# Kernel optimization log

Measured on AMD Instinct MI355X. Metric: run time of the kernel, lower is better.

## Reference

```python
import jax, jax.numpy as jnp
import numpy as np

B, D, H = 4096, 1024, 1024


def setup_inputs() -> dict:
    key = jax.random.key(0)
    ks = jax.random.split(key, 20)
    s_in = 1.0 / np.sqrt(D)
    s_hid = 1.0 / np.sqrt(H)
    inp = {
        "x_t": jax.random.normal(ks[0], (B, D), dtype=jnp.float32),
        "h_t_1": jax.random.normal(ks[1], (B, H), dtype=jnp.float32),
        "c_t_1": jax.random.normal(ks[2], (B, H), dtype=jnp.float32),
        # input-to-hidden weights (nn.Linear: y = x @ W.T + b), stacked i,f,o,z
        "W": jax.random.uniform(ks[3], (4, H, D), minval=-s_in, maxval=s_in, dtype=jnp.float32),
        "bW": jax.random.uniform(ks[4], (4, H), minval=-s_in, maxval=s_in, dtype=jnp.float32),
        # hidden-to-hidden weights, stacked i,f,o,z
        "U": jax.random.uniform(ks[5], (4, H, H), minval=-s_hid, maxval=s_hid, dtype=jnp.float32),
        "bU": jax.random.uniform(ks[6], (4, H), minval=-s_hid, maxval=s_hid, dtype=jnp.float32),
    }
    return inp


def reference(x_t, h_t_1, c_t_1, W, bW, U, bU):
    # Two stacked GEMMs: [B,D]x[4,H,D] -> [4,B,H], [B,H]x[4,H,H] -> [4,B,H]
    gx = jnp.einsum("bd,ghd->gbh", x_t, W) + bW[:, None, :]
    gh = jnp.einsum("bh,gkh->gbk", h_t_1, U) + bU[:, None, :]
    g = gx + gh  # [4, B, H] pre-activations for i, f, o, z
    i = jax.nn.sigmoid(g[0])
    f = jax.nn.sigmoid(g[1])
    o = jax.nn.sigmoid(g[2])
    z = jnp.tanh(g[3])
    c_t = i * z + f * c_t_1
    h_t = o * jnp.tanh(c_t)
    return (h_t, c_t)
```

## Files before the change

kernel.cpp:

```cpp
#include <hip/hip_runtime.h>
#include <math.h>

#define Mm 4096
#define Nn 4096
#define Kk 2048

typedef __bf16 bf16x8 __attribute__((ext_vector_type(8)));
typedef float f32x4 __attribute__((ext_vector_type(4)));

__device__ __forceinline__ unsigned short f2bf(float f) {
    union { float f; unsigned u; } v; v.f = f;
    unsigned r = v.u + 0x7FFFu + ((v.u >> 16) & 1u);
    return (unsigned short)(r >> 16);
}

__device__ __forceinline__ float fast_tanh(float x) {
    return 1.f - 2.f / (1.f + __expf(2.f * x));
}

__global__ void pack_bf16(const float* __restrict__ x, const float* __restrict__ h,
                          const float* __restrict__ W, const float* __restrict__ U,
                          const float* __restrict__ bW, const float* __restrict__ bU,
                          unsigned short* __restrict__ Xc, unsigned short* __restrict__ Wc,
                          float* __restrict__ bsum) {
    if (blockIdx.x == 0) {
#pragma unroll
        for (int j = 0; j < 16; ++j) {
            int n = threadIdx.x * 16 + j;
            int hh = n >> 2, g = n & 3;
            bsum[n] = bW[g * 1024 + hh] + bU[g * 1024 + hh];
        }
    }
    const int PER = (4096 * 1024) / 4;
    for (int t = blockIdx.x * blockDim.x + threadIdx.x; t < 4 * PER;
         t += gridDim.x * blockDim.x) {
        int region = t >> 20;
        int i = t & (PER - 1);
        int row = i >> 8;
        int c4  = i & 255;
        const float* src = (region == 0) ? x : (region == 1) ? h : (region == 2) ? W : U;
        float4 v = reinterpret_cast<const float4*>(src)[i];
        ushort4 o;
        o.x = f2bf(v.x); o.y = f2bf(v.y); o.z = f2bf(v.z); o.w = f2bf(v.w);
        if (region < 2) {
            *reinterpret_cast<ushort4*>(Xc + (size_t)row * 2048 + (region << 10) + c4 * 4) = o;
        } else {
            int g = row >> 10, hh = row & 1023;
            int np = ((hh >> 4) << 6) + (g << 4) + (hh & 15);
            *reinterpret_cast<ushort4*>(Wc + (size_t)np * 2048 + ((region & 1) << 10) + c4 * 4) = o;
        }
    }
}

__device__ __forceinline__ void gl16(const void* g, void* l) {
    __builtin_amdgcn_global_load_lds(
        (const __attribute__((address_space(1))) void*)g,
        (__attribute__((address_space(3))) void*)l, 16, 0, 0);
}

#define A_OFF(p, ah) (((p) * 2 + (ah)) * 16384)
#define B_OFF(p, hb) (65536 + ((p) * 2 + (hb)) * 16384)

__global__ __launch_bounds__(512, 2) void gemm_8ph(const unsigned short* __restrict__ A,
                                                   const unsigned short* __restrict__ Bw,
                                                   const float* __restrict__ bsum,
                                                   const float* __restrict__ cprev,
                                                   float* __restrict__ out) {
    extern __shared__ char lds[];
    const int tid = threadIdx.x, lane = tid & 63, wave = tid >> 6;
    const int wm = wave >> 2, wn = wave & 3;

    const int bid = blockIdx.x;
    const int swz = (bid & 7) * 32 + (bid >> 3);
    const int bm = swz & 15, bn = swz >> 4;
    const size_t Crow0 = (size_t)bm * 256, Ccol0 = (size_t)bn * 256;

    const int srow = wave * 8 + (lane >> 3);
    const int scolswz = (((lane & 7) ^ (lane >> 3)) << 4);
    const char* aS[2][2];
    const char* bS[2][2];
#pragma unroll
    for (int ah = 0; ah < 2; ++ah)
#pragma unroll
        for (int j = 0; j < 2; ++j) {
            aS[ah][j] = (const char*)A  + (size_t)(Crow0 + ah * 128 + j * 64 + srow) * 4096 + scolswz;
            bS[ah][j] = (const char*)Bw + (size_t)(Ccol0 + ah * 128 + j * 64 + srow) * 4096 + scolswz;
        }

#define STG_A(p, ah, kb) do { \
        gl16(aS[ah][0] + (kb), lds + A_OFF(p, ah) + wave * 1024); \
        gl16(aS[ah][1] + (kb), lds + A_OFF(p, ah) + 8192 + wave * 1024); } while (0)
#define STG_B(p, hb, kb) do { \
        gl16(bS[hb][0] + (kb), lds + B_OFF(p, hb) + wave * 1024); \
        gl16(bS[hb][1] + (kb), lds + B_OFF(p, hb) + 8192 + wave * 1024); } while (0)

    const int arowB = (wm * 64 + (lane & 15)) * 128;
    const int browB = ((wn & 1) * 64 + (lane & 15)) * 128;
    const int c0 = (((lane >> 4) << 4)) ^ ((lane & 7) << 4);
    const int c1 = (64 + ((lane >> 4) << 4)) ^ ((lane & 7) << 4);
    const int bhb = wn >> 1;

#define LDA(p, ah, mfl, ck) (*(const bf16x8*)(lds + A_OFF(p, ah) + arowB + (mfl) * 2048 + (ck)))
#define LDB(p, nf, ck)      (*(const bf16x8*)(lds + B_OFF(p, bhb) + browB + (nf) * 2048 + (ck)))

    f32x4 acc[2][4][4] = {};

#define MFMA(a, b, c) __builtin_amdgcn_mfma_f32_16x16x32_bf16(a, b, c, 0, 0, 0)
#define MF16(ah, mfA, mfB, p00, p01, p10, p11) \
    acc[ah][mfA][0] = MFMA(p00, b00, acc[ah][mfA][0]); \
    acc[ah][mfA][1] = MFMA(p00, b10, acc[ah][mfA][1]); \
    acc[ah][mfA][2] = MFMA(p00, b20, acc[ah][mfA][2]); \
    acc[ah][mfA][3] = MFMA(p00, b30, acc[ah][mfA][3]); \
    acc[ah][mfB][0] = MFMA(p10, b00, acc[ah][mfB][0]); \
    acc[ah][mfB][1] = MFMA(p10, b10, acc[ah][mfB][1]); \
    acc[ah][mfB][2] = MFMA(p10, b20, acc[ah][mfB][2]); \
    acc[ah][mfB][3] = MFMA(p10, b30, acc[ah][mfB][3]); \
    acc[ah][mfA][0] = MFMA(p01, b01, acc[ah][mfA][0]); \
    acc[ah][mfA][1] = MFMA(p01, b11, acc[ah][mfA][1]); \
    acc[ah][mfA][2] = MFMA(p01, b21, acc[ah][mfA][2]); \
    acc[ah][mfA][3] = MFMA(p01, b31, acc[ah][mfA][3]); \
    acc[ah][mfB][0] = MFMA(p11, b01, acc[ah][mfB][0]); \
    acc[ah][mfB][1] = MFMA(p11, b11, acc[ah][mfB][1]); \
    acc[ah][mfB][2] = MFMA(p11, b21, acc[ah][mfB][2]); \
    acc[ah][mfB][3] = MFMA(p11, b31, acc[ah][mfB][3]);

#define PH_TAIL \
    __builtin_amdgcn_s_barrier(); \
    asm volatile("s_waitcnt lgkmcnt(0)" ::: "memory"); \
    __builtin_amdgcn_s_setprio(1);

#define PH_END \
    __builtin_amdgcn_s_setprio(0); \
    __builtin_amdgcn_s_barrier();

#define GROUP(p, kbA1, kbT2) \
    { \
        bf16x8 b00 = LDB(p, 0, c0), b01 = LDB(p, 0, c1), b10 = LDB(p, 1, c0), b11 = LDB(p, 1, c1); \
        bf16x8 b20 = LDB(p, 2, c0), b21 = LDB(p, 2, c1), b30 = LDB(p, 3, c0), b31 = LDB(p, 3, c1); \
        {  \
            bf16x8 a00 = LDA(p, 0, 0, c0), a01 = LDA(p, 0, 0, c1); \
            bf16x8 a10 = LDA(p, 0, 1, c0), a11 = LDA(p, 0, 1, c1); \
            STG_A((p) ^ 1, 1, kbA1); \
            PH_TAIL MF16(0, 0, 1, a00, a01, a10, a11) PH_END \
        } \
        {  \
            bf16x8 a00 = LDA(p, 0, 2, c0), a01 = LDA(p, 0, 2, c1); \
            bf16x8 a10 = LDA(p, 0, 3, c0), a11 = LDA(p, 0, 3, c1); \
            STG_B(p, 0, kbT2); \
            PH_TAIL MF16(0, 2, 3, a00, a01, a10, a11) PH_END \
        } \
        {  \
            bf16x8 a00 = LDA(p, 1, 0, c0), a01 = LDA(p, 1, 0, c1); \
            bf16x8 a10 = LDA(p, 1, 1, c0), a11 = LDA(p, 1, 1, c1); \
            STG_A(p, 0, kbT2); \
            PH_TAIL MF16(1, 0, 1, a00, a01, a10, a11) PH_END \
        } \
        {  \
            bf16x8 a00 = LDA(p, 1, 2, c0), a01 = LDA(p, 1, 2, c1); \
            bf16x8 a10 = LDA(p, 1, 3, c0), a11 = LDA(p, 1, 3, c1); \
            STG_B(p, 1, kbT2); \
            __builtin_amdgcn_s_barrier(); \
            asm volatile("s_waitcnt lgkmcnt(0)" ::: "memory"); \
            __builtin_amdgcn_s_setprio(1); \
            MF16(1, 2, 3, a00, a01, a10, a11) \
            __builtin_amdgcn_s_setprio(0); \
            asm volatile("s_waitcnt vmcnt(6)" ::: "memory"); \
            __builtin_amdgcn_s_barrier(); \
        } \
    }

    STG_B(0, 0, 0);
    STG_A(0, 0, 0);
    STG_B(0, 1, 0);
    STG_A(0, 1, 0);
    STG_B(1, 0, 128);
    STG_A(1, 0, 128);
    STG_B(1, 1, 128);
    asm volatile("s_waitcnt vmcnt(6)" ::: "memory");
    __builtin_amdgcn_s_barrier();

    for (int it = 0; it < 16; ++it) {
        const int t0 = 2 * it;
        const size_t kA1_0 = (size_t)(t0 + 1) * 128;
        const size_t kT2_0 = (t0 + 2 <= 31) ? (size_t)(t0 + 2) * 128 : 0;
        const size_t kA1_1 = kT2_0;
        const size_t kT2_1 = (t0 + 3 <= 31) ? (size_t)(t0 + 3) * 128 : 0;
        GROUP(0, kA1_0, kT2_0)
        GROUP(1, kA1_1, kT2_1)
    }

    const int hl = lane & 15;
    const int er0 = (lane >> 4) * 4;
    const int myh = (int)(Ccol0 >> 2) + wn * 16 + hl;
    const f32x4 bs = *(const f32x4*)(bsum + (size_t)myh * 4);

    float cp[2][4][4];
#pragma unroll
    for (int ah = 0; ah < 2; ++ah)
#pragma unroll
        for (int mf = 0; mf < 4; ++mf)
#pragma unroll
            for (int r = 0; r < 4; ++r)
                cp[ah][mf][r] = cprev[(size_t)(Crow0 + ah * 128 + wm * 64 + mf * 16 + er0 + r) * 1024 + myh];

#pragma unroll
    for (int ah = 0; ah < 2; ++ah)
#pragma unroll
        for (int mf = 0; mf < 4; ++mf)
#pragma unroll
            for (int r = 0; r < 4; ++r) {
                float gi = acc[ah][mf][0][r] + bs[0];
                float gf = acc[ah][mf][1][r] + bs[1];
                float go = acc[ah][mf][2][r] + bs[2];
                float gz = acc[ah][mf][3][r] + bs[3];
                float iv = 1.f / (1.f + __expf(-gi));
                float fv = 1.f / (1.f + __expf(-gf));
                float ov = 1.f / (1.f + __expf(-go));
                float zv = fast_tanh(gz);
                float cc = fmaf(iv, zv, fv * cp[ah][mf][r]);
                float hv = ov * fast_tanh(cc);
                const size_t oidx =
                    (size_t)(Crow0 + ah * 128 + wm * 64 + mf * 16 + er0 + r) * 1024 + myh;
                out[oidx] = hv;
                out[(1 << 22) + oidx] = cc;
            }

    asm volatile("s_waitcnt vmcnt(0)" ::: "memory");
}

extern "C" void kernel_launch(void* const* d_in, const int* in_sizes, int n_in,
                              void* d_out, int out_size, void* d_ws, size_t ws_size,
                              hipStream_t stream) {
    const float* x  = (const float*)d_in[0];
    const float* h  = (const float*)d_in[1];
    const float* c  = (const float*)d_in[2];
    const float* W  = (const float*)d_in[3];
    const float* bW = (const float*)d_in[4];
    const float* U  = (const float*)d_in[5];
    const float* bU = (const float*)d_in[6];
    float* out = (float*)d_out;

    char* ws = (char*)d_ws;
    unsigned short* Xc = (unsigned short*)ws;
    unsigned short* Wc = (unsigned short*)(ws + ((size_t)16 << 20));
    float* bsum = (float*)(ws + ((size_t)32 << 20));

    (void)hipFuncSetAttribute((const void*)gemm_8ph,
                              hipFuncAttributeMaxDynamicSharedMemorySize, 131072);

    hipLaunchKernelGGL(pack_bf16, dim3(2048), dim3(256), 0, stream,
                       x, h, W, U, bW, bU, Xc, Wc, bsum);
    hipLaunchKernelGGL(gemm_8ph, dim3(256), dim3(512), 131072, stream,
                       Xc, Wc, bsum, c, out);
}
```

Baseline: 84.83 us.

## Double-buffer A fragments in registers and halve barriers per MFMA phase

Restructures the inner GROUP schedule so LDS reads of the next A fragments are issued before the current phase's MFMAs, ping-ponging between two register sets. This lets LDS latency overlap with matrix math. The two barriers per phase become one, and the per-phase lgkmcnt(0) wait is replaced by a vmcnt(6) wait plus sched_barrier. It costs more registers, and dropping the explicit LDS wait leaves correctness to the compiler inserting waits before dependent MFMAs. The barrier reduction may also race the LDS stores against the reads.

```diff
diff --git a/kernel.cpp b/kernel.cpp
--- a/kernel.cpp
+++ b/kernel.cpp
@@ -124,49 +124,52 @@
     acc[ah][mfB][2] = MFMA(p11, b21, acc[ah][mfB][2]); \
     acc[ah][mfB][3] = MFMA(p11, b31, acc[ah][mfB][3]);
 
-#define PH_TAIL \
-    __builtin_amdgcn_s_barrier(); \
-    asm volatile("s_waitcnt lgkmcnt(0)" ::: "memory"); \
-    __builtin_amdgcn_s_setprio(1);
-
-#define PH_END \
-    __builtin_amdgcn_s_setprio(0); \
-    __builtin_amdgcn_s_barrier();
+#define SGB0 __builtin_amdgcn_sched_barrier(0)
+#define SBAR __builtin_amdgcn_s_barrier()
 
 #define GROUP(p, kbA1, kbT2) \
     { \
+         \
         bf16x8 b00 = LDB(p, 0, c0), b01 = LDB(p, 0, c1), b10 = LDB(p, 1, c0), b11 = LDB(p, 1, c1); \
         bf16x8 b20 = LDB(p, 2, c0), b21 = LDB(p, 2, c1), b30 = LDB(p, 3, c0), b31 = LDB(p, 3, c1); \
-        {  \
-            bf16x8 a00 = LDA(p, 0, 0, c0), a01 = LDA(p, 0, 0, c1); \
-            bf16x8 a10 = LDA(p, 0, 1, c0), a11 = LDA(p, 0, 1, c1); \
-            STG_A((p) ^ 1, 1, kbA1); \
-            PH_TAIL MF16(0, 0, 1, a00, a01, a10, a11) PH_END \
-        } \
-        {  \
-            bf16x8 a00 = LDA(p, 0, 2, c0), a01 = LDA(p, 0, 2, c1); \
-            bf16x8 a10 = LDA(p, 0, 3, c0), a11 = LDA(p, 0, 3, c1); \
-            STG_B(p, 0, kbT2); \
-            PH_TAIL MF16(0, 2, 3, a00, a01, a10, a11) PH_END \
-        } \
-        {  \
-            bf16x8 a00 = LDA(p, 1, 0, c0), a01 = LDA(p, 1, 0, c1); \
-            bf16x8 a10 = LDA(p, 1, 1, c0), a11 = LDA(p, 1, 1, c1); \
-            STG_A(p, 0, kbT2); \
-            PH_TAIL MF16(1, 0, 1, a00, a01, a10, a11) PH_END \
-        } \
-        {  \
-            bf16x8 a00 = LDA(p, 1, 2, c0), a01 = LDA(p, 1, 2, c1); \
-            bf16x8 a10 = LDA(p, 1, 3, c0), a11 = LDA(p, 1, 3, c1); \
-            STG_B(p, 1, kbT2); \
-            __builtin_amdgcn_s_barrier(); \
-            asm volatile("s_waitcnt lgkmcnt(0)" ::: "memory"); \
-            __builtin_amdgcn_s_setprio(1); \
-            MF16(1, 2, 3, a00, a01, a10, a11) \
-            __builtin_amdgcn_s_setprio(0); \
-            asm volatile("s_waitcnt vmcnt(6)" ::: "memory"); \
-            __builtin_amdgcn_s_barrier(); \
-        } \
+        bf16x8 a0 = LDA(p, 0, 0, c0), a1 = LDA(p, 0, 0, c1); \
+        bf16x8 a2 = LDA(p, 0, 1, c0), a3 = LDA(p, 0, 1, c1); \
+        bf16x8 n0 = LDA(p, 0, 2, c0), n1 = LDA(p, 0, 2, c1); \
+        bf16x8 n2 = LDA(p, 0, 3, c0), n3 = LDA(p, 0, 3, c1); \
+        STG_A((p) ^ 1, 1, kbA1); \
+        asm volatile("s_waitcnt vmcnt(6)" ::: "memory"); \
+        SGB0; \
+        __builtin_amdgcn_s_setprio(1); \
+        MF16(0, 0, 1, a0, a1, a2, a3) \
+        __builtin_amdgcn_s_setprio(0); \
+        SBAR; \
+         \
+        a0 = LDA(p, 1, 0, c0); a1 = LDA(p, 1, 0, c1); \
+        a2 = LDA(p, 1, 1, c0); a3 = LDA(p, 1, 1, c1); \
+        STG_B(p, 0, kbT2); \
+        asm volatile("s_waitcnt vmcnt(6)" ::: "memory"); \
+        SGB0; \
+        __builtin_amdgcn_s_setprio(1); \
+        MF16(0, 2, 3, n0, n1, n2, n3) \
+        __builtin_amdgcn_s_setprio(0); \
+        SBAR; \
+         \
+        n0 = LDA(p, 1, 2, c0); n1 = LDA(p, 1, 2, c1); \
+        n2 = LDA(p, 1, 3, c0); n3 = LDA(p, 1, 3, c1); \
+        STG_A(p, 0, kbT2); \
+        asm volatile("s_waitcnt vmcnt(6)" ::: "memory"); \
+        SGB0; \
+        __builtin_amdgcn_s_setprio(1); \
+        MF16(1, 0, 1, a0, a1, a2, a3) \
+        __builtin_amdgcn_s_setprio(0); \
+        SBAR; \
+         \
+        STG_B(p, 1, kbT2); \
+        SGB0; \
+        __builtin_amdgcn_s_setprio(1); \
+        MF16(1, 2, 3, n0, n1, n2, n3) \
+        __builtin_amdgcn_s_setprio(0); \
+        SBAR; \
     }
 
     STG_B(0, 0, 0);
```

New measurement: 83.95 us. About the same (-1.0%).
